# Performance work log

Measured on AMD Instinct MI355X. Metric: run time of the kernel, lower is better.

Reference implementation:

```python
import jax, jax.numpy as jnp
import numpy as np

ABS_DIM, HIDDEN, ACTION_DIM, N_TASKS, B = 512, 512, 18, 16, 8192
W_SCALE = 0.001


def setup_inputs() -> dict:
    key = jax.random.key(0)
    k1, k2, k3, k4, k5 = jax.random.split(key, 5)
    x = jax.random.normal(k1, (B, ABS_DIM), dtype=jnp.float32)
    task_id = jax.random.randint(k2, (B,), 0, N_TASKS)
    action = jax.random.randint(k3, (B,), 0, ACTION_DIM)
    # Per-task weight banks (MultiLinear), w_scale=0.001
    W1 = jax.random.normal(k4, (N_TASKS, ABS_DIM, HIDDEN), dtype=jnp.float32) * W_SCALE
    b1 = jnp.zeros((N_TASKS, HIDDEN), dtype=jnp.float32)
    W2 = jax.random.normal(k5, (N_TASKS, HIDDEN, ACTION_DIM), dtype=jnp.float32) * W_SCALE
    b2 = jnp.zeros((N_TASKS, ACTION_DIM), dtype=jnp.float32)
    return {"x": x, "task_id": task_id, "action": action,
            "W1": W1, "b1": b1, "W2": W2, "b2": b2}


def _multi_linear(x, W, b, task_id):
    # x: [B, din], W: [T, din, dout], b: [T, dout]
    # Compute all experts then select per-sample (dense grouped-GEMM form).
    y_all = jnp.einsum('bi,tio->tbo', x, W) + b[:, None, :]  # [T, B, dout]
    rows = jnp.arange(x.shape[0])
    return y_all[task_id, rows]  # [B, dout]


def reference(x, task_id, action, W1, b1, W2, b2):
    h = jax.nn.relu(_multi_linear(x, W1, b1, task_id))          # [B, H]
    logits = _multi_linear(h, W2, b2, task_id)                  # [B, A]
    logprobs = jax.nn.log_softmax(logits, axis=1)               # [B, A]
    rows = jnp.arange(x.shape[0])
    log_pi_a = logprobs[rows, action][:, None]                  # [B, 1]
    ent = -jnp.sum(jnp.exp(logprobs) * logprobs, axis=1, keepdims=True)  # [B, 1]
    # forward output: concat of log_pi_a and entropy (action passes through)
    return jnp.concatenate([log_pi_a, ent], axis=1)             # [B, 2]
```

## Files before the change

### kernel.cpp

```cpp
#include <hip/hip_runtime.h>
#include <hip/hip_bf16.h>

#define B_N   8192
#define DIN   512
#define DH    512
#define NACT  18
#define NTASK 16
#define BM    64
#define GBN   128
#define BK    64
#define PJ    20
#define NSLOT 640

typedef __attribute__((ext_vector_type(8))) short  short8v;
typedef __attribute__((ext_vector_type(8))) unsigned short ushort8v;
typedef __attribute__((ext_vector_type(4))) float  float4v;
typedef __attribute__((ext_vector_type(2))) float  float2v;

typedef const __attribute__((address_space(1))) void* gas_ptr;
typedef __attribute__((address_space(3))) void* las_ptr;

__device__ __forceinline__ unsigned short f2bf(float f) {
  union { float f; unsigned int u; } c; c.f = f;
  unsigned int u = c.u;
  u += 0x7fffu + ((u >> 16) & 1u);
  return (unsigned short)(u >> 16);
}

__global__ __launch_bounds__(256) void k_prep(
    const float* __restrict__ W1, const float* __restrict__ W2,
    const int* __restrict__ task_id,
    short* __restrict__ W1T, short* __restrict__ W2T,
    int* __restrict__ tbl, int* __restrict__ rowidx) {
  __shared__ __align__(16) short ldsA[64][72];
  __shared__ float ldsB[64 * 19];
  __shared__ int s_cnt[NTASK], s_cur[NTASK];
  int bx = blockIdx.x, tid = threadIdx.x;

  if (bx == 0) {
    if (tid < NTASK) s_cnt[tid] = 0;
    __syncthreads();
    for (int i = tid; i < B_N; i += 256) atomicAdd(&s_cnt[task_id[i]], 1);
    __syncthreads();
    if (tid == 0) {
      int acc = 0;
#pragma unroll
      for (int t = 0; t < NTASK; ++t) {
        int c = s_cnt[t];
        tbl[t] = c; tbl[16 + t] = acc; s_cur[t] = acc;
        acc += c;
      }
    }
    __syncthreads();
    for (int i = tid; i < B_N; i += 256) {
      int t = task_id[i];
      rowidx[atomicAdd(&s_cur[t], 1)] = i;
    }
  } else if (bx <= 1024) {
    int u = bx - 1;
    int nb = u & 7, kb = (u >> 3) & 7, t = u >> 6;
    int r = tid >> 2, c16 = (tid & 3) << 4;
    const float* src = W1 + ((size_t)t * DIN + (size_t)(kb * 64 + r)) * DH + nb * 64 + c16;
#pragma unroll
    for (int p = 0; p < 4; ++p) {
      float4v v = *(const float4v*)(src + p * 4);
#pragma unroll
      for (int i = 0; i < 4; ++i) ldsA[c16 + p * 4 + i][r] = (short)f2bf(v[i]);
    }
    __syncthreads();
    int n = tid >> 2, k16 = (tid & 3) << 4;
    short* dst = W1T + ((size_t)t * DH + nb * 64 + n) * DIN + kb * 64 + k16;
    *(ushort8v*)dst       = *(ushort8v*)&ldsA[n][k16];
    *(ushort8v*)(dst + 8) = *(ushort8v*)&ldsA[n][k16 + 8];
  } else {
    int u = bx - 1025;
    int t = u >> 3, k0 = (u & 7) * 64;
    for (int i = tid; i < 64 * NACT; i += 256) {
      int kk = i / NACT, j = i - kk * NACT;
      ldsB[kk * 19 + j] = W2[((size_t)t * DIN + k0 + kk) * NACT + j];
    }
    __syncthreads();
    for (int o = tid; o < 32 * 64; o += 256) {
      int j = o >> 6, kk = o & 63;
      float val = (j < NACT) ? ldsB[kk * 19 + j] : 0.0f;
      W2T[((size_t)t * 32 + j) * DIN + k0 + kk] = (short)f2bf(val);
    }
  }
}

__global__ __launch_bounds__(256, 2) void k_gemm1(
    const float* __restrict__ x, const float* __restrict__ bias1,
    const short* __restrict__ W1T, const short* __restrict__ W2Tg,
    const int* __restrict__ tbl, const int* __restrict__ rowidx,
    float* __restrict__ pbuf) {
  __shared__ __align__(16) short sA[2][64 * 72];
  __shared__ __align__(16) short sB[2][GBN * BK];
  __shared__ __align__(16) short sH[BM * GBN];
  __shared__ __align__(16) short sW2[32 * GBN];
  __shared__ int s_rows[64];
  int tid = threadIdx.x, lane = tid & 63, wave = tid >> 6;

  int b = blockIdx.x;
  int t = -1, rel = 0;
  if (b < NSLOT) {
    int r = b & 7, q = b >> 3;
    int n0t = (tbl[r] + 63) >> 6, n1t = (tbl[r + 8] + 63) >> 6;
    if (q < 4 * n0t) { t = r; rel = q; }
    else if (q < 4 * (n0t + n1t)) { t = r + 8; rel = q - 4 * n0t; }
    else return;
  } else {
    int j = b - NSLOT;
    for (int r = 0; r < 8; ++r) {
      int n0t = (tbl[r] + 63) >> 6, n1t = (tbl[r + 8] + 63) >> 6;
      int P = 4 * (n0t + n1t);
      int S = (P > 80) ? (P - 80) : 0;
      if (j < S) {
        int q = 80 + j;
        if (q < 4 * n0t) { t = r; rel = q; }
        else { t = r + 8; rel = q - 4 * n0t; }
        break;
      }
      j -= S;
    }
    if (t < 0) return;
  }
  int itile = rel >> 2, cs = rel & 3;
  int cnt_t = tbl[t], off_t = tbl[16 + t];
  int row0 = off_t + itile * 64;
  int mcnt = cnt_t - itile * 64; if (mcnt > 64) mcnt = 64;
  int n0 = cs * GBN;
  int wm = wave >> 1, wn = wave & 1;

  if (tid < 64) {
    int idx = row0 + tid;
    if (idx > B_N - 1) idx = B_N - 1;
    s_rows[tid] = rowidx[idx];
  }
#pragma unroll
  for (int it = 0; it < 2; ++it) {
    int ch = it * 256 + tid;
    int j = ch >> 4, c2 = ch & 15;
    ushort8v w = *(const ushort8v*)(W2Tg + ((size_t)t * 32 + j) * DIN + n0 + c2 * 8);
    *(ushort8v*)&sW2[(j * 16 + (c2 ^ (j & 7))) * 8] = w;
  }
  __syncthreads();

  int arow = tid >> 2, akc = (tid & 3) << 4;
  const float* xrow = x + (size_t)s_rows[arow] * DIN + akc;
  const short* Bbase = W1T + ((size_t)t * DH + n0) * DIN;

#define STAGE_B(buf, k0e)                                                    \
  _Pragma("unroll") for (int it = 0; it < 4; ++it) {                         \
    int ch = it * 256 + tid; int row = ch >> 3, cc = ch & 7;                 \
    int sc = cc ^ (row & 7);                                                 \
    __builtin_amdgcn_global_load_lds(                                        \
        (gas_ptr)(const void*)(Bbase + (size_t)row * DIN + (k0e) + sc * 8),  \
        (las_ptr)(void*)(&sB[buf][ch * 8]), 16, 0, 0);                       \
  }
#define STAGE_A(buf, k0e) {                                                  \
    const float* xs_ = xrow + (k0e);                                         \
    float4v v0 = *(const float4v*)xs_;                                       \
    float4v v1 = *(const float4v*)(xs_ + 4);                                 \
    float4v v2 = *(const float4v*)(xs_ + 8);                                 \
    float4v v3 = *(const float4v*)(xs_ + 12);                                \
    ushort8v p0, p1;                                                         \
    _Pragma("unroll") for (int i_ = 0; i_ < 4; ++i_) {                       \
      p0[i_] = f2bf(v0[i_]); p0[4 + i_] = f2bf(v1[i_]);                      \
      p1[i_] = f2bf(v2[i_]); p1[4 + i_] = f2bf(v3[i_]); }                    \
    *(ushort8v*)&sA[buf][arow * 72 + akc] = p0;                              \
    *(ushort8v*)&sA[buf][arow * 72 + akc + 8] = p1; }

  STAGE_B(0, 0)
  STAGE_A(0, 0)
  asm volatile("s_waitcnt vmcnt(0)" ::: "memory");
  __syncthreads();

  float4v acc[2][4];
#pragma unroll
  for (int i = 0; i < 2; ++i)
#pragma unroll
    for (int j = 0; j < 4; ++j) acc[i][j] = (float4v)0.0f;

  for (int step = 0; step < 8; ++step) {
    int p = step & 1;
    if (step < 7) {
      STAGE_B(p ^ 1, (step + 1) * BK)
      STAGE_A(p ^ 1, (step + 1) * BK)
    }
#pragma unroll
    for (int ks = 0; ks < 2; ++ks) {
      short8v a[2], bfr[4];
#pragma unroll
      for (int fm = 0; fm < 2; ++fm) {
        int r = wm * 32 + fm * 16 + (lane & 15);
        int c = ks * 4 + (lane >> 4);
        a[fm] = *(const short8v*)&sA[p][r * 72 + c * 8];
      }
#pragma unroll
      for (int fn = 0; fn < 4; ++fn) {
        int r = wn * 64 + fn * 16 + (lane & 15);
        int c = (ks * 4 + (lane >> 4)) ^ (r & 7);
        bfr[fn] = *(const short8v*)&sB[p][r * BK + c * 8];
      }
#pragma unroll
      for (int fm = 0; fm < 2; ++fm)
#pragma unroll
        for (int fn = 0; fn < 4; ++fn)
          acc[fm][fn] = __builtin_amdgcn_mfma_f32_16x16x32_bf16(a[fm], bfr[fn], acc[fm][fn], 0, 0, 0);
    }
    asm volatile("s_waitcnt vmcnt(0)" ::: "memory");
    __syncthreads();
  }

  float bias[4];
#pragma unroll
  for (int fn = 0; fn < 4; ++fn)
    bias[fn] = bias1[t * DH + n0 + wn * 64 + fn * 16 + (lane & 15)];
#pragma unroll
  for (int fn = 0; fn < 4; ++fn) {
    int n = wn * 64 + fn * 16 + (lane & 15);
#pragma unroll
    for (int fm = 0; fm < 2; ++fm) {
#pragma unroll
      for (int r = 0; r < 4; ++r) {
        int m = wm * 32 + fm * 16 + ((lane >> 4) << 2) + r;
        float v = fmaxf(acc[fm][fn][r] + bias[fn], 0.0f);
        *(short*)((char*)sH + m * 256 + (((n >> 3) ^ (m & 7)) << 4) + ((n & 7) << 1)) =
            (short)f2bf(v);
      }
    }
  }
  __syncthreads();

  float4v acc2[2];
  acc2[0] = (float4v)0.0f; acc2[1] = (float4v)0.0f;
#pragma unroll
  for (int ks = 0; ks < 4; ++ks) {
    int mrow = wave * 16 + (lane & 15);
    int ca = (ks * 4 + (lane >> 4)) ^ (mrow & 7);
    short8v af = *(const short8v*)((char*)sH + mrow * 256 + (ca << 4));
#pragma unroll
    for (int fn = 0; fn < 2; ++fn) {
      int j = fn * 16 + (lane & 15);
      int cb = (ks * 4 + (lane >> 4)) ^ (j & 7);
      short8v bf = *(const short8v*)&sW2[(j * 16 + cb) * 8];
      acc2[fn] = __builtin_amdgcn_mfma_f32_16x16x32_bf16(af, bf, acc2[fn], 0, 0, 0);
    }
  }
#pragma unroll
  for (int fn = 0; fn < 2; ++fn) {
#pragma unroll
    for (int r = 0; r < 4; ++r) {
      int m = wave * 16 + ((lane >> 4) << 2) + r;
      int j = fn * 16 + (lane & 15);
      if (m < mcnt && j < PJ)
        pbuf[((size_t)cs * B_N + row0 + m) * PJ + j] = acc2[fn][r];
    }
  }
#undef STAGE_B
#undef STAGE_A
}

__global__ __launch_bounds__(256) void k_soft(
    const float* __restrict__ pbuf, const float* __restrict__ bias2,
    const int* __restrict__ task_id, const int* __restrict__ action,
    const int* __restrict__ rowidx, float* __restrict__ out) {
  __shared__ float acc[256 * PJ];
  int tid = threadIdx.x;
  int base = blockIdx.x * 256;
#pragma unroll
  for (int it = 0; it < 5; ++it) {
    int idx = it * 256 + tid;
    int row = idx / 5, j4 = idx - row * 5;
    float4v s = (float4v)0.0f;
#pragma unroll
    for (int c = 0; c < 4; ++c)
      s += *(const float4v*)&pbuf[((size_t)c * B_N + base + row) * PJ + j4 * 4];
    *(float4v*)&acc[row * PJ + j4 * 4] = s;
  }
  __syncthreads();

  int srow = base + tid;
  int orig = rowidx[srow];
  int t = task_id[orig], act = action[orig];
  float lg[NACT];
#pragma unroll
  for (int j = 0; j < NACT; ++j) lg[j] = acc[tid * PJ + j] + bias2[t * NACT + j];
  float mx = lg[0];
#pragma unroll
  for (int j = 1; j < NACT; ++j) mx = fmaxf(mx, lg[j]);
  float s1 = 0.0f, s2 = 0.0f, la = 0.0f;
#pragma unroll
  for (int j = 0; j < NACT; ++j) {
    float e = __expf(lg[j] - mx);
    s1 += e; s2 += e * lg[j];
    la = (j == act) ? lg[j] : la;
  }
  float logZ = __logf(s1);
  float2v o;
  o[0] = la - mx - logZ;
  o[1] = (mx + logZ) - s2 / s1;
  *(float2v*)(out + (size_t)orig * 2) = o;
}

extern "C" void kernel_launch(void* const* d_in, const int* in_sizes, int n_in,
                              void* d_out, int out_size, void* d_ws, size_t ws_size,
                              hipStream_t stream) {
  const float* x       = (const float*)d_in[0];
  const int*   task_id = (const int*)d_in[1];
  const int*   action  = (const int*)d_in[2];
  const float* W1      = (const float*)d_in[3];
  const float* b1      = (const float*)d_in[4];
  const float* W2      = (const float*)d_in[5];
  const float* b2      = (const float*)d_in[6];
  float* out = (float*)d_out;

  char* ws = (char*)d_ws;
  int* tbl    = (int*)ws;
  int* rowidx = (int*)(ws + 4096);
  size_t off = 36864;
  short* W1T  = (short*)(ws + off);  off += (size_t)NTASK * DH * DIN * 2;
  short* W2T  = (short*)(ws + off);  off += (size_t)NTASK * 32 * DIN * 2;
  float* pbuf = (float*)(ws + off);

  k_prep<<<1153, 256, 0, stream>>>(W1, W2, task_id, W1T, W2T, tbl, rowidx);
  k_gemm1<<<NSLOT + 576, 256, 0, stream>>>(x, b1, W1T, W2T, tbl, rowidx, pbuf);
  k_soft<<<32, 256, 0, stream>>>(pbuf, b2, task_id, action, rowidx, out);
}
```

Baseline: 48.91 us.

## Fuse weight conversion into GEMM and softmax into last-arriving tile block

Drops the separate W1/W2 transpose-and-convert pass. The GEMM kernel now reads fp32 W1 and W2 directly and converts them to bf16 in registers before writing to LDS. The separate softmax kernel is also removed: a per-tile atomic counter lets the last of the four column-slice blocks reduce the partial logits and write log-prob and entropy. Prep shrinks to a single-block bucketing kernel. The cost is that every tile block re-reads and re-converts fp32 weights (twice the bytes, no async global-to-LDS loads), and synchronous register staging replaces the async path.

```diff
diff --git a/kernel.cpp b/kernel.cpp
--- a/kernel.cpp
+++ b/kernel.cpp
@@ -17,87 +17,54 @@
 typedef __attribute__((ext_vector_type(4))) float  float4v;
 typedef __attribute__((ext_vector_type(2))) float  float2v;
 
-typedef const __attribute__((address_space(1))) void* gas_ptr;
-typedef __attribute__((address_space(3))) void* las_ptr;
-
-__device__ __forceinline__ unsigned short f2bf(float f) {
-  union { float f; unsigned int u; } c; c.f = f;
-  unsigned int u = c.u;
-  u += 0x7fffu + ((u >> 16) & 1u);
-  return (unsigned short)(u >> 16);
-}
-
-__global__ __launch_bounds__(256) void k_prep(
-    const float* __restrict__ W1, const float* __restrict__ W2,
+__device__ __forceinline__ unsigned short bfbits(float f) {
+  __hip_bfloat16 b = __float2bfloat16(f);
+  return *reinterpret_cast<unsigned short*>(&b);
+}
+
+__global__ __launch_bounds__(1024) void k_prep(
     const int* __restrict__ task_id,
-    short* __restrict__ W1T, short* __restrict__ W2T,
-    int* __restrict__ tbl, int* __restrict__ rowidx) {
-  __shared__ __align__(16) short ldsA[64][72];
-  __shared__ float ldsB[64 * 19];
-  __shared__ int s_cnt[NTASK], s_cur[NTASK];
-  int bx = blockIdx.x, tid = threadIdx.x;
-
-  if (bx == 0) {
-    if (tid < NTASK) s_cnt[tid] = 0;
-    __syncthreads();
-    for (int i = tid; i < B_N; i += 256) atomicAdd(&s_cnt[task_id[i]], 1);
-    __syncthreads();
-    if (tid == 0) {
-      int acc = 0;
-#pragma unroll
-      for (int t = 0; t < NTASK; ++t) {
-        int c = s_cnt[t];
-        tbl[t] = c; tbl[16 + t] = acc; s_cur[t] = acc;
-        acc += c;
-      }
-    }
-    __syncthreads();
-    for (int i = tid; i < B_N; i += 256) {
-      int t = task_id[i];
-      rowidx[atomicAdd(&s_cur[t], 1)] = i;
-    }
-  } else if (bx <= 1024) {
-    int u = bx - 1;
-    int nb = u & 7, kb = (u >> 3) & 7, t = u >> 6;
-    int r = tid >> 2, c16 = (tid & 3) << 4;
-    const float* src = W1 + ((size_t)t * DIN + (size_t)(kb * 64 + r)) * DH + nb * 64 + c16;
-#pragma unroll
-    for (int p = 0; p < 4; ++p) {
-      float4v v = *(const float4v*)(src + p * 4);
-#pragma unroll
-      for (int i = 0; i < 4; ++i) ldsA[c16 + p * 4 + i][r] = (short)f2bf(v[i]);
-    }
-    __syncthreads();
-    int n = tid >> 2, k16 = (tid & 3) << 4;
-    short* dst = W1T + ((size_t)t * DH + nb * 64 + n) * DIN + kb * 64 + k16;
-    *(ushort8v*)dst       = *(ushort8v*)&ldsA[n][k16];
-    *(ushort8v*)(dst + 8) = *(ushort8v*)&ldsA[n][k16 + 8];
-  } else {
-    int u = bx - 1025;
-    int t = u >> 3, k0 = (u & 7) * 64;
-    for (int i = tid; i < 64 * NACT; i += 256) {
-      int kk = i / NACT, j = i - kk * NACT;
-      ldsB[kk * 19 + j] = W2[((size_t)t * DIN + k0 + kk) * NACT + j];
-    }
-    __syncthreads();
-    for (int o = tid; o < 32 * 64; o += 256) {
-      int j = o >> 6, kk = o & 63;
-      float val = (j < NACT) ? ldsB[kk * 19 + j] : 0.0f;
-      W2T[((size_t)t * 32 + j) * DIN + k0 + kk] = (short)f2bf(val);
-    }
+    int* __restrict__ tbl, int* __restrict__ rowidx, int* __restrict__ tile_cnt) {
+  __shared__ int c4[4][NTASK];
+  __shared__ int cur4[4][NTASK];
+  int tid = threadIdx.x;
+  if (tid < 64) ((int*)c4)[tid] = 0;
+  for (int i = tid; i < NTASK * 128; i += 1024) tile_cnt[i] = 0;
+  __syncthreads();
+  for (int i = tid; i < B_N; i += 1024)
+    atomicAdd(&c4[i >> 11][task_id[i]], 1);
+  __syncthreads();
+  if (tid == 0) {
+    int acc = 0;
+    for (int t = 0; t < NTASK; ++t) {
+      int c = c4[0][t] + c4[1][t] + c4[2][t] + c4[3][t];
+      tbl[t] = c; tbl[16 + t] = acc;
+      int o = acc;
+#pragma unroll
+      for (int q = 0; q < 4; ++q) { cur4[q][t] = o; o += c4[q][t]; }
+      acc += c;
+    }
+  }
+  __syncthreads();
+  for (int i = tid; i < B_N; i += 1024) {
+    int t = task_id[i];
+    rowidx[atomicAdd(&cur4[i >> 11][t], 1)] = i;
   }
 }
 
 __global__ __launch_bounds__(256, 2) void k_gemm1(
     const float* __restrict__ x, const float* __restrict__ bias1,
-    const short* __restrict__ W1T, const short* __restrict__ W2Tg,
+    const float* __restrict__ W1, const float* __restrict__ W2,
+    const float* __restrict__ bias2, const int* __restrict__ action,
     const int* __restrict__ tbl, const int* __restrict__ rowidx,
-    float* __restrict__ pbuf) {
-  __shared__ __align__(16) short sA[2][64 * 72];
+    int* __restrict__ tile_cnt, float* __restrict__ pbuf,
+    float* __restrict__ out) {
+  __shared__ __align__(16) short sA[2][BM * 72];
   __shared__ __align__(16) short sB[2][GBN * BK];
   __shared__ __align__(16) short sH[BM * GBN];
   __shared__ __align__(16) short sW2[32 * GBN];
   __shared__ int s_rows[64];
+  __shared__ int s_last;
   int tid = threadIdx.x, lane = tid & 63, wave = tid >> 6;
 
   int b = blockIdx.x;
@@ -138,41 +105,45 @@
   }
 #pragma unroll
   for (int it = 0; it < 2; ++it) {
-    int ch = it * 256 + tid;
-    int j = ch >> 4, c2 = ch & 15;
-    ushort8v w = *(const ushort8v*)(W2Tg + ((size_t)t * 32 + j) * DIN + n0 + c2 * 8);
-    *(ushort8v*)&sW2[(j * 16 + (c2 ^ (j & 7))) * 8] = w;
+    int slot = it * 256 + tid;
+    int j = slot & 31, kc = slot >> 5;
+    int jc = (j < NACT) ? j : 0;
+    const float* src = W2 + ((size_t)t * DIN + n0 + kc * 8) * NACT + jc;
+    ushort8v pk;
+#pragma unroll
+    for (int i = 0; i < 8; ++i) {
+      float v = src[(size_t)i * NACT];
+      pk[i] = (j < NACT) ? bfbits(v) : (unsigned short)0;
+    }
+    *(ushort8v*)((char*)sW2 + (j * 16 + (kc ^ (j & 7))) * 16) = pk;
   }
   __syncthreads();
 
   int arow = tid >> 2, akc = (tid & 3) << 4;
   const float* xrow = x + (size_t)s_rows[arow] * DIN + akc;
-  const short* Bbase = W1T + ((size_t)t * DH + n0) * DIN;
-
-#define STAGE_B(buf, k0e)                                                    \
-  _Pragma("unroll") for (int it = 0; it < 4; ++it) {                         \
-    int ch = it * 256 + tid; int row = ch >> 3, cc = ch & 7;                 \
-    int sc = cc ^ (row & 7);                                                 \
-    __builtin_amdgcn_global_load_lds(                                        \
-        (gas_ptr)(const void*)(Bbase + (size_t)row * DIN + (k0e) + sc * 8),  \
-        (las_ptr)(void*)(&sB[buf][ch * 8]), 16, 0, 0);                       \
-  }
-#define STAGE_A(buf, k0e) {                                                  \
-    const float* xs_ = xrow + (k0e);                                         \
-    float4v v0 = *(const float4v*)xs_;                                       \
-    float4v v1 = *(const float4v*)(xs_ + 4);                                 \
-    float4v v2 = *(const float4v*)(xs_ + 8);                                 \
-    float4v v3 = *(const float4v*)(xs_ + 12);                                \
-    ushort8v p0, p1;                                                         \
-    _Pragma("unroll") for (int i_ = 0; i_ < 4; ++i_) {                       \
-      p0[i_] = f2bf(v0[i_]); p0[4 + i_] = f2bf(v1[i_]);                      \
-      p1[i_] = f2bf(v2[i_]); p1[4 + i_] = f2bf(v3[i_]); }                    \
-    *(ushort8v*)&sA[buf][arow * 72 + akc] = p0;                              \
+  int bk8 = tid >> 5, bn4 = tid & 31;
+  const float* w1base = W1 + (size_t)t * DIN * DH + n0 + bn4 * 4;
+
+  float4v La[4], Lb[8];
+#define LOAD_A(k0e) { _Pragma("unroll") for (int j_ = 0; j_ < 4; ++j_) \
+    La[j_] = *(const float4v*)(xrow + (k0e) + j_ * 4); }
+#define WRITE_A(buf) { ushort8v p0, p1;                                   \
+    _Pragma("unroll") for (int i_ = 0; i_ < 4; ++i_) {                    \
+      p0[i_] = bfbits(La[0][i_]); p0[4 + i_] = bfbits(La[1][i_]);         \
+      p1[i_] = bfbits(La[2][i_]); p1[4 + i_] = bfbits(La[3][i_]); }       \
+    *(ushort8v*)&sA[buf][arow * 72 + akc] = p0;                           \
     *(ushort8v*)&sA[buf][arow * 72 + akc + 8] = p1; }
-
-  STAGE_B(0, 0)
-  STAGE_A(0, 0)
-  asm volatile("s_waitcnt vmcnt(0)" ::: "memory");
+#define LOAD_B(k0e) { _Pragma("unroll") for (int j_ = 0; j_ < 8; ++j_) \
+    Lb[j_] = *(const float4v*)(w1base + (size_t)((k0e) + bk8 * 8 + j_) * DH); }
+#define WRITE_B(buf) { _Pragma("unroll") for (int c_ = 0; c_ < 4; ++c_) { \
+    int n_ = bn4 * 4 + c_;                                                \
+    ushort8v pk;                                                          \
+    _Pragma("unroll") for (int j_ = 0; j_ < 8; ++j_)                      \
+      pk[j_] = bfbits(Lb[j_][c_]);                                        \
+    *(ushort8v*)((char*)sB[buf] + n_ * 128 + ((bk8 ^ (n_ & 7)) << 4)) = pk; } }
+
+  LOAD_A(0) LOAD_B(0)
+  WRITE_A(0) WRITE_B(0)
   __syncthreads();
 
   float4v acc[2][4];
@@ -183,10 +154,7 @@
 
   for (int step = 0; step < 8; ++step) {
     int p = step & 1;
-    if (step < 7) {
-      STAGE_B(p ^ 1, (step + 1) * BK)
-      STAGE_A(p ^ 1, (step + 1) * BK)
-    }
+    if (step < 7) { LOAD_A((step + 1) * BK) LOAD_B((step + 1) * BK) }
 #pragma unroll
     for (int ks = 0; ks < 2; ++ks) {
       short8v a[2], bfr[4];
@@ -208,7 +176,7 @@
         for (int fn = 0; fn < 4; ++fn)
           acc[fm][fn] = __builtin_amdgcn_mfma_f32_16x16x32_bf16(a[fm], bfr[fn], acc[fm][fn], 0, 0, 0);
     }
-    asm volatile("s_waitcnt vmcnt(0)" ::: "memory");
+    if (step < 7) { WRITE_A(p ^ 1) WRITE_B(p ^ 1) }
     __syncthreads();
   }
 
@@ -226,7 +194,7 @@
         int m = wm * 32 + fm * 16 + ((lane >> 4) << 2) + r;
         float v = fmaxf(acc[fm][fn][r] + bias[fn], 0.0f);
         *(short*)((char*)sH + m * 256 + (((n >> 3) ^ (m & 7)) << 4) + ((n & 7) << 1)) =
-            (short)f2bf(v);
+            (short)bfbits(v);
       }
     }
   }
@@ -257,50 +225,49 @@
         pbuf[((size_t)cs * B_N + row0 + m) * PJ + j] = acc2[fn][r];
     }
   }
-#undef STAGE_B
-#undef STAGE_A
-}
-
-__global__ __launch_bounds__(256) void k_soft(
-    const float* __restrict__ pbuf, const float* __restrict__ bias2,
-    const int* __restrict__ task_id, const int* __restrict__ action,
-    const int* __restrict__ rowidx, float* __restrict__ out) {
-  __shared__ float acc[256 * PJ];
-  int tid = threadIdx.x;
-  int base = blockIdx.x * 256;
-#pragma unroll
-  for (int it = 0; it < 5; ++it) {
-    int idx = it * 256 + tid;
-    int row = idx / 5, j4 = idx - row * 5;
-    float4v s = (float4v)0.0f;
-#pragma unroll
-    for (int c = 0; c < 4; ++c)
-      s += *(const float4v*)&pbuf[((size_t)c * B_N + base + row) * PJ + j4 * 4];
-    *(float4v*)&acc[row * PJ + j4 * 4] = s;
-  }
-  __syncthreads();
-
-  int srow = base + tid;
-  int orig = rowidx[srow];
-  int t = task_id[orig], act = action[orig];
-  float lg[NACT];
-#pragma unroll
-  for (int j = 0; j < NACT; ++j) lg[j] = acc[tid * PJ + j] + bias2[t * NACT + j];
-  float mx = lg[0];
-#pragma unroll
-  for (int j = 1; j < NACT; ++j) mx = fmaxf(mx, lg[j]);
-  float s1 = 0.0f, s2 = 0.0f, la = 0.0f;
-#pragma unroll
-  for (int j = 0; j < NACT; ++j) {
-    float e = __expf(lg[j] - mx);
-    s1 += e; s2 += e * lg[j];
-    la = (j == act) ? lg[j] : la;
-  }
-  float logZ = __logf(s1);
-  float2v o;
-  o[0] = la - mx - logZ;
-  o[1] = (mx + logZ) - s2 / s1;
-  *(float2v*)(out + (size_t)orig * 2) = o;
+
+  __threadfence();
+  __syncthreads();
+  if (tid == 0) {
+    int key = (t << 7) | itile;
+    s_last = (atomicAdd(&tile_cnt[key], 1) == 3) ? 1 : 0;
+  }
+  __syncthreads();
+  if (s_last) {
+    __threadfence();
+    if (tid < mcnt) {
+      int m = tid, orig = s_rows[m];
+      int act = action[orig];
+      float lg[NACT];
+#pragma unroll
+      for (int j = 0; j < NACT; ++j) {
+        float v = bias2[t * NACT + j];
+#pragma unroll
+        for (int c = 0; c < 4; ++c)
+          v += pbuf[((size_t)c * B_N + row0 + m) * PJ + j];
+        lg[j] = v;
+      }
+      float mx = lg[0];
+#pragma unroll
+      for (int j = 1; j < NACT; ++j) mx = fmaxf(mx, lg[j]);
+      float s1 = 0.0f, s2 = 0.0f, la = 0.0f;
+#pragma unroll
+      for (int j = 0; j < NACT; ++j) {
+        float e = __expf(lg[j] - mx);
+        s1 += e; s2 += e * lg[j];
+        la = (j == act) ? lg[j] : la;
+      }
+      float logZ = __logf(s1);
+      float2v o;
+      o[0] = la - mx - logZ;
+      o[1] = (mx + logZ) - s2 / s1;
+      *(float2v*)(out + (size_t)orig * 2) = o;
+    }
+  }
+#undef LOAD_A
+#undef WRITE_A
+#undef LOAD_B
+#undef WRITE_B
 }
 
 extern "C" void kernel_launch(void* const* d_in, const int* in_sizes, int n_in,
@@ -316,14 +283,12 @@
   float* out = (float*)d_out;
 
   char* ws = (char*)d_ws;
-  int* tbl    = (int*)ws;
-  int* rowidx = (int*)(ws + 4096);
-  size_t off = 36864;
-  short* W1T  = (short*)(ws + off);  off += (size_t)NTASK * DH * DIN * 2;
-  short* W2T  = (short*)(ws + off);  off += (size_t)NTASK * 32 * DIN * 2;
-  float* pbuf = (float*)(ws + off);
-
-  k_prep<<<1153, 256, 0, stream>>>(W1, W2, task_id, W1T, W2T, tbl, rowidx);
-  k_gemm1<<<NSLOT + 576, 256, 0, stream>>>(x, b1, W1T, W2T, tbl, rowidx, pbuf);
-  k_soft<<<32, 256, 0, stream>>>(pbuf, b2, task_id, action, rowidx, out);
-}
+  int* tbl      = (int*)ws;
+  int* rowidx   = (int*)(ws + 4096);
+  int* tile_cnt = (int*)(ws + 36864);
+  float* pbuf   = (float*)(ws + 45056);
+
+  k_prep<<<1, 1024, 0, stream>>>(task_id, tbl, rowidx, tile_cnt);
+  k_gemm1<<<NSLOT + 576, 256, 0, stream>>>(x, b1, W1, W2, b2, action,
+                                           tbl, rowidx, tile_cnt, pbuf, out);
+}
```

New measurement: 104.0 us. 2.13x slower.
